# Performance work log

Measured on AMD Instinct MI355X. Metric: run time of the kernel, lower is better.

The kernel has to match this reference:

```python
import jax, jax.numpy as jnp
import numpy as np
from jax import lax

B, CIN, COUT, H, W = 8, 128, 128, 128, 128
HID = COUT // 2  # expansion 0.5
K = 3            # kernel size
PAD = 1


def silu(v):
    return v * jax.nn.sigmoid(v)


def base_conv1x1(x, w, s, b):
    # 1x1 conv (no bias) + folded-BN affine (scale s, bias b) + SiLU
    y = jnp.einsum('bchw,oc->bohw', x, w)
    return silu(y * s[None, :, None, None] + b[None, :, None, None])


def bilinear_gather(img, py, px):
    Hin, Win = img.shape[1], img.shape[2]
    y0 = jnp.floor(py)
    x0 = jnp.floor(px)
    wy = py - y0
    wx = px - x0

    def corner(yc, xc):
        valid = (yc >= 0) & (yc <= Hin - 1) & (xc >= 0) & (xc <= Win - 1)
        yi = jnp.clip(yc, 0, Hin - 1).astype(jnp.int32)
        xi = jnp.clip(xc, 0, Win - 1).astype(jnp.int32)
        v = img[:, yi, xi]  # [C, Kk, H, W]
        return v * valid[None].astype(img.dtype)

    v00 = corner(y0, x0)
    v01 = corner(y0, x0 + 1)
    v10 = corner(y0 + 1, x0)
    v11 = corner(y0 + 1, x0 + 1)
    wy = wy[None]
    wx = wx[None]
    return (v00 * (1 - wy) * (1 - wx) + v01 * (1 - wy) * wx
            + v10 * wy * (1 - wx) + v11 * wy * wx)


def deform_conv_depthwise(x, off_w, off_b, dw):
    # x: [B, C, H, W]; off_w: [2*K*K, C, 3, 3]; dw: [C, K, K] (depthwise, groups=C)
    b, c, h, w = x.shape
    off = lax.conv_general_dilated(
        x, off_w, window_strides=(1, 1), padding=((PAD, PAD), (PAD, PAD)),
        dimension_numbers=('NCHW', 'OIHW', 'NCHW'))
    off = off + off_b[None, :, None, None]
    off = off.reshape(b, K * K, 2, h, w)  # torchvision: (dy, dx) per tap
    dy, dx = off[:, :, 0], off[:, :, 1]   # [B, 9, H, W]

    ky = jnp.repeat(jnp.arange(K, dtype=x.dtype), K)  # [9]
    kx = jnp.tile(jnp.arange(K, dtype=x.dtype), K)
    yy = jnp.arange(h, dtype=x.dtype)[None, :, None]  # [1, H, 1]
    xx = jnp.arange(w, dtype=x.dtype)[None, None, :]
    py = yy + ky[:, None, None] - PAD  # [9, H, W]
    px = xx + kx[:, None, None] - PAD
    py = py[None] + dy  # [B, 9, H, W]
    px = px[None] + dx

    sampled = jax.vmap(bilinear_gather)(x, py, px)  # [B, C, 9, H, W]
    return jnp.einsum('bckhw,ck->bchw', sampled, dw.reshape(c, K * K))


def setup_inputs() -> dict:
    key = jax.random.key(0)
    ks = jax.random.split(key, 12)
    f = jnp.float32
    inp = {
        'x': jax.random.normal(ks[0], (B, CIN, H, W), f),
        'w1': jax.random.normal(ks[1], (HID, CIN), f) * 0.05,
        's1': jnp.ones((HID,), f), 'b1': jnp.zeros((HID,), f),
        'w2': jax.random.normal(ks[2], (HID, CIN), f) * 0.05,
        's2': jnp.ones((HID,), f), 'b2': jnp.zeros((HID,), f),
        'w3': jax.random.normal(ks[3], (COUT, 2 * HID), f) * 0.05,
        's3': jnp.ones((COUT,), f), 'b3': jnp.zeros((COUT,), f),
        'off_w': jax.random.normal(ks[4], (2 * K * K, HID, K, K), f) * 0.01,
        'off_b': jnp.zeros((2 * K * K,), f),
        'dw': jax.random.normal(ks[5], (HID, K, K), f) * 0.1,
    }
    return inp


def reference(x, w1, s1, b1, w2, s2, b2, w3, s3, b3, off_w, off_b, dw):
    x1 = base_conv1x1(x, w1, s1, b1)          # [B, HID, H, W]
    x2 = base_conv1x1(x, w2, s2, b2)          # [B, HID, H, W]
    x1 = deform_conv_depthwise(x1, off_w, off_b, dw)
    xc = jnp.concatenate([x1, x2], axis=1)    # [B, 2*HID, H, W]
    return base_conv1x1(xc, w3, s3, b3)       # [B, COUT, H, W]
```

## Files before the change

kernel.cpp:

```cpp
#include <hip/hip_runtime.h>

typedef unsigned short u16;
typedef unsigned int   u32;
typedef unsigned char  u8;

#define BB    8
#define CINC  128
#define HIDC  64
#define COUTC 128
#define HH    128
#define WWD   128
#define HWN   16384
#define NPOS  (BB*HWN)

typedef __attribute__((ext_vector_type(8))) short bf16x8;
typedef __attribute__((ext_vector_type(4))) float f32x4;

__device__ __forceinline__ float b2f(u16 u){
    union { u32 i; float f; } v; v.i = ((u32)u) << 16; return v.f;
}
__device__ __forceinline__ u16 f2b(float f){
    union { float f; u32 i; } v; v.f = f;
    u32 i = v.i;
    i += 0x7fffu + ((i >> 16) & 1u);
    return (u16)(i >> 16);
}
__device__ __forceinline__ float blo(u32 u){
    union { u32 i; float f; } v; v.i = u << 16; return v.f;
}
__device__ __forceinline__ float bhi(u32 u){
    union { u32 i; float f; } v; v.i = u & 0xFFFF0000u; return v.f;
}
__device__ __forceinline__ float silu(float y){
    return y / (1.f + __expf(-y));
}

template<bool ISB>
__device__ __forceinline__ float ldp(const void* p, int i){
    if (ISB) return b2f(((const u16*)p)[i]);
    return ((const float*)p)[i];
}

template<bool ISB>
__device__ __forceinline__ void k0_body(
    const void* w1, const void* s1, const void* b1,
    const void* w2, const void* s2, const void* b2,
    const void* w3, const void* s3, const void* b3,
    const void* offw, const void* offb, const void* dw,
    u16* __restrict__ wbc, u16* __restrict__ wb3,
    float* __restrict__ bfc, float* __restrict__ bf3,
    u16* __restrict__ wA, float* __restrict__ ob32, float* __restrict__ dwfT)
{
    int t = blockIdx.x*256 + threadIdx.x;
    if (t < 8192){
        wbc[t] = f2b(ldp<ISB>(w1,t) * ldp<ISB>(s1,t>>7));
    } else if (t < 16384){
        int u = t - 8192;
        wbc[t] = f2b(ldp<ISB>(w2,u) * ldp<ISB>(s2,u>>7));
    }
    if (t < 16384){
        wb3[t] = f2b(ldp<ISB>(w3,t) * ldp<ISB>(s3,t>>7));
    }
    if (t < 18432){
        int set  = t / 9216, rem = t % 9216;
        int tap  = rem / 1024; int rem2 = rem % 1024;
        int chunk= rem2 >> 9;  int rem3 = rem2 & 511;
        int lane = rem3 >> 3;  int jp   = rem3 & 7;
        int jg   = set*16 + (lane & 15);
        int c    = chunk*32 + (lane>>4)*8 + jp;
        float v  = (jg < 18) ? ldp<ISB>(offw, (jg*HIDC + c)*9 + tap) : 0.f;
        wA[t] = f2b(v);
    }
    if (t < HIDC)  bfc[t]      = ldp<ISB>(b1,t);
    if (t >= HIDC && t < 2*HIDC) bfc[t] = ldp<ISB>(b2,t-HIDC);
    if (t < COUTC) bf3[t] = ldp<ISB>(b3,t);
    if (t < 32)    ob32[t] = (t < 18) ? ldp<ISB>(offb,t) : 0.f;
    if (t < HIDC*9){
        int c = t / 9, k = t % 9;
        dwfT[k*HIDC + c] = ldp<ISB>(dw,t);
    }
}

__global__ __launch_bounds__(256) void k0_prep(
    const void* w1, const void* s1, const void* b1,
    const void* w2, const void* s2, const void* b2,
    const void* w3, const void* s3, const void* b3,
    const void* offw, const void* offb, const void* dw,
    u16* wbc, u16* wb3, float* bfc, float* bf3,
    u16* wA, float* ob32, float* dwfT)
{
    bool isb = (((const u32*)s1)[0] == 0x3F803F80u);
    if (isb) k0_body<true >(w1,s1,b1,w2,s2,b2,w3,s3,b3,offw,offb,dw,wbc,wb3,bfc,bf3,wA,ob32,dwfT);
    else     k0_body<false>(w1,s1,b1,w2,s2,b2,w3,s3,b3,offw,offb,dw,wbc,wb3,bfc,bf3,wA,ob32,dwfT);
}

template<bool ISB>
__device__ __forceinline__ void k1_body(const void* __restrict__ xv,
    const u16* __restrict__ wbc, const float* __restrict__ bfc,
    u16* __restrict__ x1, u16* __restrict__ x2, u8* __restrict__ sx8)
{
    const int posb = blockIdx.x*64;
    const int bidx = posb >> 14;
    const int hwb  = posb & (HWN-1);

    {
        const int R  = threadIdx.x >> 2;
        const int qq = threadIdx.x & 3;
        u32* dst = (u32*)(sx8 + R*272 + qq*64);
        if (ISB){
            const u16* r0 = (const u16*)xv + (size_t)bidx*CINC*HWN + (size_t)(2*R)*HWN + hwb + qq*16;
            const u16* r1 = r0 + HWN;
            uint4 a0 = *(const uint4*)(r0);
            uint4 a1 = *(const uint4*)(r0 + 8);
            uint4 c0 = *(const uint4*)(r1);
            uint4 c1 = *(const uint4*)(r1 + 8);
            u32 A[8] = {a0.x,a0.y,a0.z,a0.w,a1.x,a1.y,a1.z,a1.w};
            u32 C[8] = {c0.x,c0.y,c0.z,c0.w,c1.x,c1.y,c1.z,c1.w};
            #pragma unroll
            for (int k = 0; k < 8; ++k){
                dst[2*k]   = (A[k] & 0xFFFFu) | (C[k] << 16);
                dst[2*k+1] = (A[k] >> 16)     | (C[k] & 0xFFFF0000u);
            }
        } else {
            const float* r0 = (const float*)xv + (size_t)bidx*CINC*HWN + (size_t)(2*R)*HWN + hwb + qq*16;
            const float* r1 = r0 + HWN;
            #pragma unroll
            for (int k = 0; k < 8; ++k){
                float2 f0 = *(const float2*)(r0 + 2*k);
                float2 f1 = *(const float2*)(r1 + 2*k);
                dst[2*k]   = (u32)f2b(f0.x) | ((u32)f2b(f1.x) << 16);
                dst[2*k+1] = (u32)f2b(f0.y) | ((u32)f2b(f1.y) << 16);
            }
        }
    }
    __syncthreads();

    const int w    = threadIdx.x >> 6;
    const int lane = threadIdx.x & 63;
    const int n    = lane & 15;
    const int quad = lane >> 4;

    bf16x8 wf[2][4];
    #pragma unroll
    for (int m = 0; m < 2; ++m)
        #pragma unroll
        for (int t = 0; t < 4; ++t)
            wf[m][t] = *(const bf16x8*)(wbc + (size_t)(w*32 + m*16 + n)*CINC + t*32 + quad*8);

    f32x4 acc[2][4];
    #pragma unroll
    for (int m = 0; m < 2; ++m)
        #pragma unroll
        for (int s = 0; s < 4; ++s) acc[m][s] = (f32x4){0.f,0.f,0.f,0.f};

    #pragma unroll
    for (int t = 0; t < 4; ++t){
        #pragma unroll
        for (int sub = 0; sub < 4; ++sub){
            union { u32 u[4]; bf16x8 v; } bb;
            #pragma unroll
            for (int jp = 0; jp < 4; ++jp)
                bb.u[jp] = *(const u32*)(sx8 + (t*16 + quad*4 + jp)*272 + (sub*16 + n)*4);
            acc[0][sub] = __builtin_amdgcn_mfma_f32_16x16x32_bf16(wf[0][t], bb.v, acc[0][sub], 0,0,0);
            acc[1][sub] = __builtin_amdgcn_mfma_f32_16x16x32_bf16(wf[1][t], bb.v, acc[1][sub], 0,0,0);
        }
    }

    #pragma unroll
    for (int m = 0; m < 2; ++m){
        const int ob = w*32 + m*16 + quad*4;
        float4 bi = *(const float4*)(bfc + ob);
        u16* dbuf = (ob < 64) ? x1 : x2;
        const int oo = ob & 63;
        #pragma unroll
        for (int sub = 0; sub < 4; ++sub){
            const u32 lo = (u32)f2b(silu(acc[m][sub][0] + bi.x))
                         | ((u32)f2b(silu(acc[m][sub][1] + bi.y)) << 16);
            const u32 hi = (u32)f2b(silu(acc[m][sub][2] + bi.z))
                         | ((u32)f2b(silu(acc[m][sub][3] + bi.w)) << 16);
            *(uint2*)(dbuf + (size_t)(posb + sub*16 + n)*HIDC + oo) = make_uint2(lo, hi);
        }
    }
}

__global__ __launch_bounds__(256) void k1_mfma(const void* x, const u32* s1probe,
    const u16* wbc, const float* bfc, u16* x1, u16* x2)
{
    __shared__ __align__(16) u8 sx8[64*272];
    bool isb = (s1probe[0] == 0x3F803F80u);
    if (isb) k1_body<true >(x, wbc, bfc, x1, x2, sx8);
    else     k1_body<false>(x, wbc, bfc, x1, x2, sx8);
}

__global__ __launch_bounds__(256, 3) void k23_fused(const u16* __restrict__ x1,
    const u16* __restrict__ wA, const float* __restrict__ ob32,
    const float* __restrict__ dwfT, u16* __restrict__ x1d)
{
    __shared__ float s_dwf[576];
    __shared__ float s_offs[64*21];
    __shared__ int   s_offi[64*12];
    __shared__ __align__(16) float4 s_facs[64*9];

    const int tid  = threadIdx.x;
    if (tid < 144)
        *(float4*)(s_dwf + tid*4) = *(const float4*)(dwfT + tid*4);

    const int w    = tid >> 6;
    const int lane = tid & 63;
    const int n    = lane & 15;
    const int quad = lane >> 4;
    const int posb = blockIdx.x*64;
    const int b    = posb >> 14;
    const u16* bbase = x1 + (size_t)b*HWN*HIDC;

    {
        const int posbase = posb + w*16;
        const int hw  = posbase & (HWN-1);
        const int y   = hw >> 7;
        const int x0  = hw & (WWD-1);
        const int xb  = x0 + n - 1;

        f32x4 acc0 = (f32x4){0.f,0.f,0.f,0.f};
        f32x4 acc1 = (f32x4){0.f,0.f,0.f,0.f};

        #pragma unroll
        for (int ky = 0; ky < 3; ++ky){
            int ys = y + ky - 1;
            if ((unsigned)ys >= HH) continue;
            const u16* rowp = bbase + (size_t)ys*WWD*HIDC;
            #pragma unroll
            for (int kx = 0; kx < 3; ++kx){
                int  xs  = xb + kx;
                int  xcl = min(max(xs, 0), WWD-1);
                bool vx  = ((unsigned)xs < WWD);
                const int tap = ky*3 + kx;
                #pragma unroll
                for (int ch = 0; ch < 2; ++ch){
                    bf16x8 bfr = *(const bf16x8*)(rowp + xcl*HIDC + ch*32 + quad*8);
                    if (!vx) bfr = (bf16x8){0,0,0,0,0,0,0,0};
                    bf16x8 a0 = *(const bf16x8*)(wA + ((0*9 + tap)*2 + ch)*512 + lane*8);
                    bf16x8 a1 = *(const bf16x8*)(wA + ((1*9 + tap)*2 + ch)*512 + lane*8);
                    acc0 = __builtin_amdgcn_mfma_f32_16x16x32_bf16(a0, bfr, acc0, 0,0,0);
                    acc1 = __builtin_amdgcn_mfma_f32_16x16x32_bf16(a1, bfr, acc1, 0,0,0);
                }
            }
        }
        const int pl = w*16 + n;
        #pragma unroll
        for (int r = 0; r < 4; ++r){
            int j0 = quad*4 + r;
            s_offs[pl*21 + j0] = acc0[r] + ob32[j0];
            int j1 = 16 + quad*4 + r;
            if (j1 < 18)
                s_offs[pl*21 + j1] = acc1[r] + ob32[j1];
        }
    }

    #pragma unroll
    for (int t = 0; t < 3; ++t){
        int task = t*64 + lane;
        if (task < 144){
            int pll = task / 9;
            int k   = task - pll*9;
            int pl  = w*16 + pll;
            int pos = posb + pl;
            int hw = pos & (HWN-1);
            int y  = hw >> 7, x = hw & (WWD-1);
            float dy = s_offs[pl*21 + 2*k];
            float dx = s_offs[pl*21 + 2*k + 1];
            float py = (float)(y + k/3 - 1) + dy;
            float px = (float)(x + k%3 - 1) + dx;
            float fy = floorf(py), fx = floorf(px);
            float wy = py - fy,    wx = px - fx;
            int y0 = (int)fy, x0i = (int)fx;
            float vy0 = ((unsigned)y0      < HH)  ? 1.f : 0.f;
            float vy1 = ((unsigned)(y0+1)  < HH)  ? 1.f : 0.f;
            float vx0 = ((unsigned)x0i     < WWD) ? 1.f : 0.f;
            float vx1 = ((unsigned)(x0i+1) < WWD) ? 1.f : 0.f;
            int yc0 = min(max(y0,   0), HH-1),  yc1 = min(max(y0+1, 0), HH-1);
            int xc0 = min(max(x0i,  0), WWD-1), xc1 = min(max(x0i+1, 0), WWD-1);
            float wy1 = 1.f - wy, wx1 = 1.f - wx;
            float4 w4;
            w4.x = wy1*wx1*vy0*vx0;
            w4.y = wy1*wx *vy0*vx1;
            w4.z = wy *wx1*vy1*vx0;
            w4.w = wy *wx *vy1*vx1;
            int o0 = (yc0*WWD + xc0)*HIDC;
            int sx = (xc1 != xc0) ? 1 : 0;
            int sy = (yc1 != yc0) ? 1 : 0;
            s_offi[pl*12 + k] = o0 | (sx<<20) | (sy<<21);
            s_facs[pl*9 + k]  = w4;
        }
    }
    __syncthreads();

    const int cg = lane & 7;
    const u32* xb32 = (const u32*)bbase + cg*4;
    #pragma unroll
    for (int it = 0; it < 2; ++it){
        const int posl = w*16 + it*8 + (lane >> 3);
        const int pos  = posb + posl;
        float acc[8];
        #pragma unroll
        for (int j = 0; j < 8; ++j) acc[j] = 0.f;
        #pragma unroll
        for (int k = 0; k < 9; ++k){
            const int    pk = s_offi[posl*12 + k];
            const float4 f  = s_facs[posl*9 + k];
            const float4 d0 = *(const float4*)(s_dwf + k*HIDC + cg*8);
            const float4 d1 = *(const float4*)(s_dwf + k*HIDC + cg*8 + 4);
            const int o0  = (pk & 0xFFFFF) >> 1;
            const int dxs = (pk & (1<<20)) ? (HIDC>>1)       : 0;
            const int dys = (pk & (1<<21)) ? ((WWD*HIDC)>>1) : 0;
            const uint4 q00 = *(const uint4*)(xb32 + o0);
            const uint4 q01 = *(const uint4*)(xb32 + o0 + dxs);
            const uint4 q10 = *(const uint4*)(xb32 + o0 + dys);
            const uint4 q11 = *(const uint4*)(xb32 + o0 + dys + dxs);
            #define BIL(J, C00, C01, C10, C11, DLO, DHI) { \
                float slo = blo(C00)*f.x + blo(C01)*f.y + blo(C10)*f.z + blo(C11)*f.w; \
                float shi = bhi(C00)*f.x + bhi(C01)*f.y + bhi(C10)*f.z + bhi(C11)*f.w; \
                acc[2*(J)]   += slo*(DLO); \
                acc[2*(J)+1] += shi*(DHI); }
            BIL(0, q00.x, q01.x, q10.x, q11.x, d0.x, d0.y)
            BIL(1, q00.y, q01.y, q10.y, q11.y, d0.z, d0.w)
            BIL(2, q00.z, q01.z, q10.z, q11.z, d1.x, d1.y)
            BIL(3, q00.w, q01.w, q10.w, q11.w, d1.z, d1.w)
            #undef BIL
        }
        const u32 r0 = (u32)f2b(acc[0]) | ((u32)f2b(acc[1]) << 16);
        const u32 r1 = (u32)f2b(acc[2]) | ((u32)f2b(acc[3]) << 16);
        const u32 r2 = (u32)f2b(acc[4]) | ((u32)f2b(acc[5]) << 16);
        const u32 r3 = (u32)f2b(acc[6]) | ((u32)f2b(acc[7]) << 16);
        *(uint4*)(x1d + (size_t)pos*HIDC + cg*8) = make_uint4(r0, r1, r2, r3);
    }
}

template<bool ISB>
__device__ __forceinline__ void k4_body(const u16* __restrict__ x1d,
    const u16* __restrict__ x2,
    const u16* __restrict__ wb3, const float* __restrict__ bf3,
    void* __restrict__ out)
{
    const int posb = blockIdx.x*64;
    const int bidx = posb >> 14;
    const int hwb  = posb & (HWN-1);
    const int w    = threadIdx.x >> 6;
    const int lane = threadIdx.x & 63;
    const int n    = lane & 15;
    const int quad = lane >> 4;

    bf16x8 wf[2][4];
    #pragma unroll
    for (int m = 0; m < 2; ++m)
        #pragma unroll
        for (int t = 0; t < 4; ++t)
            wf[m][t] = *(const bf16x8*)(wb3 + (size_t)(w*32 + m*16 + n)*CINC + t*32 + quad*8);

    f32x4 acc[2][4];
    #pragma unroll
    for (int m = 0; m < 2; ++m)
        #pragma unroll
        for (int s = 0; s < 4; ++s) acc[m][s] = (f32x4){0.f,0.f,0.f,0.f};

    #pragma unroll
    for (int t = 0; t < 4; ++t){
        const u16* src = (t < 2) ? x1d : x2;
        #pragma unroll
        for (int sub = 0; sub < 4; ++sub){
            bf16x8 bfr = *(const bf16x8*)(src + (size_t)(posb + sub*16 + n)*HIDC + (t&1)*32 + quad*8);
            acc[0][sub] = __builtin_amdgcn_mfma_f32_16x16x32_bf16(wf[0][t], bfr, acc[0][sub], 0,0,0);
            acc[1][sub] = __builtin_amdgcn_mfma_f32_16x16x32_bf16(wf[1][t], bfr, acc[1][sub], 0,0,0);
        }
    }

    u16*   ob16 = (u16*)  out + (size_t)bidx*COUTC*HWN + hwb;
    float* obf  = (float*)out + (size_t)bidx*COUTC*HWN + hwb;
    #pragma unroll
    for (int m = 0; m < 2; ++m){
        const int ob = w*32 + m*16 + quad*4;
        float4 bi = *(const float4*)(bf3 + ob);
        #pragma unroll
        for (int sub = 0; sub < 4; ++sub){
            const int pp = sub*16 + n;
            #pragma unroll
            for (int r = 0; r < 4; ++r){
                const float bv = (r==0)?bi.x:(r==1)?bi.y:(r==2)?bi.z:bi.w;
                const float v = silu(acc[m][sub][r] + bv);
                if (ISB) ob16[(size_t)(ob+r)*HWN + pp] = f2b(v);
                else     obf [(size_t)(ob+r)*HWN + pp] = v;
            }
        }
    }
}

__global__ __launch_bounds__(256) void k4_mfma(const u16* x1d, const u16* x2,
    const u32* s1probe, const u16* wb3, const float* bf3, void* out)
{
    bool isb = (s1probe[0] == 0x3F803F80u);
    if (isb) k4_body<true >(x1d, x2, wb3, bf3, out);
    else     k4_body<false>(x1d, x2, wb3, bf3, out);
}

extern "C" void kernel_launch(void* const* d_in, const int* in_sizes, int n_in,
                              void* d_out, int out_size, void* d_ws, size_t ws_size,
                              hipStream_t stream)
{
    const void* x    = d_in[0];
    const void* w1   = d_in[1];
    const void* s1   = d_in[2];
    const void* b1   = d_in[3];
    const void* w2   = d_in[4];
    const void* s2   = d_in[5];
    const void* b2   = d_in[6];
    const void* w3   = d_in[7];
    const void* s3   = d_in[8];
    const void* b3   = d_in[9];
    const void* offw = d_in[10];
    const void* offb = d_in[11];
    const void* dw   = d_in[12];

    char* ws = (char*)d_ws;
    u16*   x1    = (u16*)  (ws + 0);
    u16*   x2    = (u16*)  (ws + 16777216);
    u16*   x1d   = (u16*)  (ws + 33554432);
    u16*   wbc   = (u16*)  (ws + 59768832);
    u16*   wb3   = (u16*)  (ws + 59801600);
    u16*   wA    = (u16*)  (ws + 59834368);
    float* dwfT  = (float*)(ws + 59871232);
    float* bfc   = (float*)(ws + 59873536);
    float* bf3   = (float*)(ws + 59874048);
    float* ob32  = (float*)(ws + 59874560);

    k0_prep<<<72, 256, 0, stream>>>(w1,s1,b1, w2,s2,b2, w3,s3,b3, offw,offb,dw,
                                    wbc, wb3, bfc, bf3, wA, ob32, dwfT);
    k1_mfma  <<<NPOS/64, 256, 0, stream>>>(x, (const u32*)s1, wbc, bfc, x1, x2);
    k23_fused<<<NPOS/64, 256, 0, stream>>>(x1, wA, ob32, dwfT, x1d);
    k4_mfma  <<<NPOS/64, 256, 0, stream>>>(x1d, x2, (const u32*)s1, wb3, bf3, d_out);
}
```

Before: 263.6 us.

## Launch deform and output kernels as single-wavefront blocks

Reworks the fused offset/deform kernel and the final 1x1 conv kernel to use 64-thread blocks, each holding one wavefront, with 4x more blocks. In the deform kernel this removes the block-wide barrier, since one wave produces and consumes its own LDS offsets. The aim is finer-grained scheduling and less barrier stalling. In exchange, per-block setup such as loading the depthwise weights into LDS is repeated more often, and there are more blocks to dispatch.

```diff
diff --git a/kernel.cpp b/kernel.cpp
--- a/kernel.cpp
+++ b/kernel.cpp
@@ -192,30 +192,31 @@
     else     k1_body<false>(x, wbc, bfc, x1, x2, sx8);
 }
 
-__global__ __launch_bounds__(256, 3) void k23_fused(const u16* __restrict__ x1,
+__global__ __launch_bounds__(64) void k23_w1(const u16* __restrict__ x1,
     const u16* __restrict__ wA, const float* __restrict__ ob32,
     const float* __restrict__ dwfT, u16* __restrict__ x1d)
 {
     __shared__ float s_dwf[576];
-    __shared__ float s_offs[64*21];
-    __shared__ int   s_offi[64*12];
-    __shared__ __align__(16) float4 s_facs[64*9];
-
-    const int tid  = threadIdx.x;
-    if (tid < 144)
-        *(float4*)(s_dwf + tid*4) = *(const float4*)(dwfT + tid*4);
-
-    const int w    = tid >> 6;
-    const int lane = tid & 63;
+    __shared__ float s_offs[16*21];
+    __shared__ int   s_offi[16*12];
+    __shared__ __align__(16) float4 s_facs[16*9];
+
+    const int lane = threadIdx.x;
     const int n    = lane & 15;
     const int quad = lane >> 4;
-    const int posb = blockIdx.x*64;
-    const int b    = posb >> 14;
+    const int posb16 = blockIdx.x*16;
+    const int b    = posb16 >> 14;
     const u16* bbase = x1 + (size_t)b*HWN*HIDC;
 
+    #pragma unroll
+    for (int i = 0; i < 3; ++i){
+        int idx = i*64 + lane;
+        if (idx < 144)
+            *(float4*)(s_dwf + idx*4) = *(const float4*)(dwfT + idx*4);
+    }
+
     {
-        const int posbase = posb + w*16;
-        const int hw  = posbase & (HWN-1);
+        const int hw  = posb16 & (HWN-1);
         const int y   = hw >> 7;
         const int x0  = hw & (WWD-1);
         const int xb  = x0 + n - 1;
@@ -245,14 +246,13 @@
                 }
             }
         }
-        const int pl = w*16 + n;
         #pragma unroll
         for (int r = 0; r < 4; ++r){
             int j0 = quad*4 + r;
-            s_offs[pl*21 + j0] = acc0[r] + ob32[j0];
+            s_offs[n*21 + j0] = acc0[r] + ob32[j0];
             int j1 = 16 + quad*4 + r;
             if (j1 < 18)
-                s_offs[pl*21 + j1] = acc1[r] + ob32[j1];
+                s_offs[n*21 + j1] = acc1[r] + ob32[j1];
         }
     }
 
@@ -260,10 +260,9 @@
     for (int t = 0; t < 3; ++t){
         int task = t*64 + lane;
         if (task < 144){
-            int pll = task / 9;
-            int k   = task - pll*9;
-            int pl  = w*16 + pll;
-            int pos = posb + pl;
+            int pl = task / 9;
+            int k  = task - pl*9;
+            int pos = posb16 + pl;
             int hw = pos & (HWN-1);
             int y  = hw >> 7, x = hw & (WWD-1);
             float dy = s_offs[pl*21 + 2*k];
@@ -292,14 +291,13 @@
             s_facs[pl*9 + k]  = w4;
         }
     }
-    __syncthreads();
 
     const int cg = lane & 7;
     const u32* xb32 = (const u32*)bbase + cg*4;
     #pragma unroll
     for (int it = 0; it < 2; ++it){
-        const int posl = w*16 + it*8 + (lane >> 3);
-        const int pos  = posb + posl;
+        const int posl = it*8 + (lane >> 3);
+        const int pos  = posb16 + posl;
         float acc[8];
         #pragma unroll
         for (int j = 0; j < 8; ++j) acc[j] = 0.f;
@@ -341,11 +339,11 @@
     const u16* __restrict__ wb3, const float* __restrict__ bf3,
     void* __restrict__ out)
 {
-    const int posb = blockIdx.x*64;
+    const int w    = blockIdx.x & 3;
+    const int posb = (blockIdx.x >> 2)*64;
     const int bidx = posb >> 14;
     const int hwb  = posb & (HWN-1);
-    const int w    = threadIdx.x >> 6;
-    const int lane = threadIdx.x & 63;
+    const int lane = threadIdx.x;
     const int n    = lane & 15;
     const int quad = lane >> 4;
 
@@ -393,7 +391,7 @@
     }
 }
 
-__global__ __launch_bounds__(256) void k4_mfma(const u16* x1d, const u16* x2,
+__global__ __launch_bounds__(64) void k4_w1(const u16* x1d, const u16* x2,
     const u32* s1probe, const u16* wb3, const float* bf3, void* out)
 {
     bool isb = (s1probe[0] == 0x3F803F80u);
@@ -433,7 +431,7 @@
 
     k0_prep<<<72, 256, 0, stream>>>(w1,s1,b1, w2,s2,b2, w3,s3,b3, offw,offb,dw,
                                     wbc, wb3, bfc, bf3, wA, ob32, dwfT);
-    k1_mfma  <<<NPOS/64, 256, 0, stream>>>(x, (const u32*)s1, wbc, bfc, x1, x2);
-    k23_fused<<<NPOS/64, 256, 0, stream>>>(x1, wA, ob32, dwfT, x1d);
-    k4_mfma  <<<NPOS/64, 256, 0, stream>>>(x1d, x2, (const u32*)s1, wb3, bf3, d_out);
-}
+    k1_mfma<<<NPOS/64, 256, 0, stream>>>(x, (const u32*)s1, wbc, bfc, x1, x2);
+    k23_w1 <<<NPOS/16, 64, 0, stream>>>(x1, wA, ob32, dwfT, x1d);
+    k4_w1  <<<(NPOS/64)*4, 64, 0, stream>>>(x1d, x2, (const u32*)s1, wb3, bf3, d_out);
+}
```

After: 232.9 us. 1.13x faster.
